# Performance work log

Hardware: AMD Instinct MI355X
Metric: run time of the kernel (lower is better)

The kernel has to match this reference:

```python
import jax, jax.numpy as jnp
import numpy as np

# Static architecture (from init_kwargs `layers`):
DAG = [0, 1, 1, 3, 3, 5]                       # parent node of linear layer i (i=1..6)
ACTS = ['tanh', 'relu', 'sigmoid', 'tanh', 'relu', 'tanh']
LEAVES = [2, 4, 6]                             # nodes never used as a parent -> combined output

V, F, H, C = 50000, 1024, 1024, 50000          # vocab, num_features, hidden_unit, num_classes
B, T = 64, 128                                 # batch, seq_len
A = 12                                         # len(actions)
N = len(DAG)


def _act(name, x):
    return {'tanh': jnp.tanh, 'relu': jax.nn.relu, 'sigmoid': jax.nn.sigmoid}[name](x)


def setup_inputs() -> dict:
    key = jax.random.key(0)
    ks = jax.random.split(key, 8)
    w = lambda k, shape: jax.random.normal(k, shape, jnp.float32) * 0.02
    return {
        'word2vec': jax.random.normal(ks[0], (V, F), jnp.float32),
        'h': jax.random.normal(ks[1], (B, H), jnp.float32),
        'batch_input': jax.random.randint(ks[2], (B, T), 0, V, jnp.int32),
        'W0': w(ks[3], (H, F)), 'b0': jnp.zeros((H,), jnp.float32),
        'Ws': w(ks[4], (N, H, H)), 'bs': jnp.zeros((N, H), jnp.float32),
        'W_out': w(ks[5], (C, H)), 'b_out': jnp.zeros((C,), jnp.float32),
        'W_sum': w(ks[6], (N, A)), 'b_sum': jnp.zeros((N,), jnp.float32),
        'actions': jnp.arange(A, dtype=jnp.float32),
    }


def reference(word2vec, h, batch_input, W0, b0, Ws, bs, W_out, b_out, W_sum, b_sum, actions):
    # softmax-weighted combine coefficients over the leaf nodes (constant across timesteps)
    weight = W_sum @ actions + b_sum                              # [N]
    clean_w = jax.nn.softmax(weight[jnp.array([l - 1 for l in LEAVES])])  # [L]

    def cell(h_t, idx):
        x = word2vec[idx]                                         # [B, F] embedding gather
        outs = {0: x @ W0.T + b0}                                 # node 0
        for i in range(1, N + 1):                                 # static DAG unroll
            prev = DAG[i - 1]
            if i == 1:
                o = h_t @ Ws[0].T + bs[0] + outs[prev]            # hidden recurrence enters node 1
            else:
                o = outs[prev] @ Ws[i - 1].T + bs[i - 1]
            outs[i] = _act(ACTS[i - 1], o)                        # dropout is identity (eval mode)
        ans = jnp.stack([outs[l] for l in LEAVES])                # [L, B, H]
        h_new = jnp.einsum('l,lbh->bh', clean_w, ans)             # weighted leaf combine
        return h_new, None

    # forward() iterates l = 1 .. T-1 (first column skipped, as in the torch code)
    h_final, _ = jax.lax.scan(cell, h, batch_input[:, 1:].T)
    return h_final @ W_out.T + b_out                              # [B, C]
```

## Files before the change

### kernel.cpp

```cpp
#include <hip/hip_runtime.h>
#include <hip/hip_bf16.h>

#define Hdim 1024
#define TST  127
#define NCLS 50000
#define POLL_GUARD (1 << 17)

typedef __attribute__((ext_vector_type(8))) short    s8v;
typedef __attribute__((ext_vector_type(4))) float    f4v;
typedef __attribute__((ext_vector_type(2))) unsigned u2v;

#define OFF_X0   0ull
#define SZ_X0    ((unsigned long long)TST * 64 * Hdim * 2ull)
#define OFF_W0B  (OFF_X0 + SZ_X0)
#define OFF_WSB  (OFF_W0B + 2097152ull)
#define OFF_ACT  (OFF_WSB + 12582912ull)
#define OFF_HB   (OFF_ACT + 524288ull)
#define OFF_FLG  (OFF_HB + 131072ull)
#define WS_NEED  (OFF_FLG + 8192ull)

__device__ __forceinline__ unsigned short f2b(float f) {
  union { float f; unsigned u; } v; v.f = f;
  return (unsigned short)((v.u + 0x7FFFu + ((v.u >> 16) & 1u)) >> 16);
}
__device__ __forceinline__ float b2f(unsigned short u) {
  union { unsigned u; float f; } v; v.u = ((unsigned)u) << 16;
  return v.f;
}
__device__ __forceinline__ float fast_tanh(float x) { return 1.f - 2.f / (__expf(2.f * x) + 1.f); }
__device__ __forceinline__ float fast_sigm(float x) { return 1.f / (1.f + __expf(-x)); }
__device__ __forceinline__ s8v pack8(const float* __restrict__ p) {
  s8v r;
#pragma unroll
  for (int i = 0; i < 8; ++i) r[i] = (short)f2b(p[i]);
  return r;
}
__device__ __forceinline__ u2v pk4(float a, float b, float c, float d) {
  u2v v;
  v[0] = (unsigned)f2b(a) | ((unsigned)f2b(b) << 16);
  v[1] = (unsigned)f2b(c) | ((unsigned)f2b(d) << 16);
  return v;
}

__device__ __forceinline__ void st_sc1_u32(unsigned* p, unsigned v) {
  asm volatile("global_store_dword %0, %1, off sc0 sc1" :: "v"(p), "v"(v) : "memory");
}
__device__ __forceinline__ void st_sc0_u32(unsigned* p, unsigned v) {
  asm volatile("global_store_dword %0, %1, off sc0" :: "v"(p), "v"(v) : "memory");
}
__device__ __forceinline__ void st_sc0_64(unsigned short* p, u2v v) {
  asm volatile("global_store_dwordx2 %0, %1, off sc0" :: "v"(p), "v"(v) : "memory");
}
__device__ __forceinline__ void wait_vm0() { asm volatile("s_waitcnt vmcnt(0)" ::: "memory"); }

__device__ __forceinline__ void pollg(const unsigned* fb, unsigned tgt) {
  const unsigned* p = fb + (threadIdx.x & 31);
  int gd = 0;
  for (;;) {
    unsigned v;
    asm volatile("global_load_dword %0, %1, off sc0 sc1\n\ts_waitcnt vmcnt(0)"
                 : "=v"(v) : "v"(p) : "memory");
    if (__all((int)(v >= tgt))) break;
    if (++gd >= POLL_GUARD) break;
  }
}

#define GL8S0(B, P) asm volatile(                                       \
  "global_load_dwordx4 %0, %8, off sc0\n\t"                             \
  "global_load_dwordx4 %1, %8, off offset:64 sc0\n\t"                   \
  "global_load_dwordx4 %2, %8, off offset:128 sc0\n\t"                  \
  "global_load_dwordx4 %3, %8, off offset:192 sc0\n\t"                  \
  "global_load_dwordx4 %4, %8, off offset:256 sc0\n\t"                  \
  "global_load_dwordx4 %5, %8, off offset:320 sc0\n\t"                  \
  "global_load_dwordx4 %6, %8, off offset:384 sc0\n\t"                  \
  "global_load_dwordx4 %7, %8, off offset:448 sc0\n\t"                  \
  "s_waitcnt vmcnt(0)"                                                  \
  : "=&v"(B[0]), "=&v"(B[1]), "=&v"(B[2]), "=&v"(B[3]),                 \
    "=&v"(B[4]), "=&v"(B[5]), "=&v"(B[6]), "=&v"(B[7])                  \
  : "v"(P) : "memory")

__global__ __launch_bounds__(256) void k_cvt(const float* __restrict__ src,
                                             unsigned short* __restrict__ dst) {
  const int i = (blockIdx.x * 256 + threadIdx.x) * 4;
  float4 v = *(const float4*)(src + i);
  ushort4 o; o.x = f2b(v.x); o.y = f2b(v.y); o.z = f2b(v.z); o.w = f2b(v.w);
  *(ushort4*)(dst + i) = o;
}

__global__ __launch_bounds__(256) void k_x0(const float* __restrict__ emb,
                                            const int* __restrict__ ids,
                                            const unsigned short* __restrict__ w0b,
                                            const float* __restrict__ b0,
                                            const float* __restrict__ bs,
                                            unsigned short* __restrict__ x0b) {
  const int t  = blockIdx.x;
  const int cb = blockIdx.y * 256;
  const int lane = threadIdx.x & 63, wvv = threadIdx.x >> 6;
  const int lc = lane & 15, lg = lane >> 4;
  const int cw = cb + wvv * 64;
  const float* erow[4];
#pragma unroll
  for (int rt = 0; rt < 4; ++rt)
    erow[rt] = emb + (size_t)ids[(rt * 16 + lc) * 128 + t + 1] * Hdim + lg * 8;
  f4v acc[4][4];
#pragma unroll
  for (int ct = 0; ct < 4; ++ct)
#pragma unroll
    for (int rt = 0; rt < 4; ++rt) acc[ct][rt] = (f4v){0.f, 0.f, 0.f, 0.f};

  for (int ks = 0; ks < 32; ++ks) {
    s8v bf[4];
#pragma unroll
    for (int rt = 0; rt < 4; ++rt) bf[rt] = pack8(erow[rt] + ks * 32);
#pragma unroll
    for (int ct = 0; ct < 4; ++ct) {
      s8v a = *(const s8v*)(w0b + (size_t)(cw + ct * 16 + lc) * Hdim + ks * 32 + lg * 8);
#pragma unroll
      for (int rt = 0; rt < 4; ++rt)
        acc[ct][rt] = __builtin_amdgcn_mfma_f32_16x16x32_bf16(a, bf[rt], acc[ct][rt], 0, 0, 0);
    }
  }
  unsigned short* xt = x0b + (size_t)t * (64 * Hdim);
#pragma unroll
  for (int ct = 0; ct < 4; ++ct) {
    const int colq = cw + ct * 16 + lg * 4;
    float4 bias = *(const float4*)(b0 + colq);
    float4 bsv  = *(const float4*)(bs + colq);
#pragma unroll
    for (int rt = 0; rt < 4; ++rt) {
      const int row = rt * 16 + lc;
      ushort4 o;
      o.x = f2b(acc[ct][rt][0] + bias.x + bsv.x);
      o.y = f2b(acc[ct][rt][1] + bias.y + bsv.y);
      o.z = f2b(acc[ct][rt][2] + bias.z + bsv.z);
      o.w = f2b(acc[ct][rt][3] + bias.w + bsv.w);
      *(ushort4*)(xt + (size_t)row * Hdim + colq) = o;
    }
  }
}

__global__ __launch_bounds__(256, 1) void k_scan(const float* __restrict__ bs,
                                                 const float* __restrict__ h_in,
                                                 const float* __restrict__ Wsum,
                                                 const float* __restrict__ bsum,
                                                 const float* __restrict__ act,
                                                 char* __restrict__ ws) {
  __shared__ float part[2][4][8][36];
  __shared__ float n2l[8][36];
  __shared__ float n4l[8][36];
  __shared__ char  pad_lds[81920];
  __shared__ int   s_info[2];

  const int tid = threadIdx.x;
  ((volatile char*)pad_lds)[tid] = (char)tid;
  asm volatile("" :: "v"((int)((volatile char*)pad_lds)[tid]));

  const int lane = tid & 63, wv = tid >> 6;
  const int lc = lane & 15, lg = lane >> 4;
  const int lr = lc & 7;
  const int lcr = lc & 7, ctx = lc >> 3;
  const int cbx = ctx * 16 + lg * 4;

  unsigned* flg_all = (unsigned*)(ws + OFF_FLG);
  unsigned* ranks   = flg_all + 1536;

  if (tid == 0) {
    unsigned x;
    asm volatile("s_getreg_b32 %0, hwreg(HW_REG_XCC_ID)" : "=s"(x));
    x &= 7u;
    unsigned rr = __hip_atomic_fetch_add(&ranks[x], 1u, __ATOMIC_RELAXED, __HIP_MEMORY_SCOPE_AGENT);
    s_info[0] = (int)x; s_info[1] = (int)rr;
  }
  __syncthreads();
  const int xcd = s_info[0];
  const int r   = s_info[1];
  if (r >= 32) return;
  const int c0w = r * 32;

  unsigned short* actX = (unsigned short*)(ws + OFF_ACT) + (size_t)xcd * 32768;
  unsigned short* hL  = actX;
  unsigned short* n1L = actX + 8192;
  unsigned short* n3L = actX + 16384;
  unsigned short* n5L = actX + 24576;
  unsigned* flgX = flg_all + xcd * 192;
  unsigned* fg0 = flgX;
  unsigned* fg2 = flgX + 64;
  unsigned* fg4 = flgX + 128;
  unsigned* fg5 = flgX + 160;
  const unsigned short* wsb = (const unsigned short*)(ws + OFF_WSB);
  const unsigned short* x0b = (const unsigned short*)(ws + OFF_X0);
  unsigned short* HB = (unsigned short*)(ws + OFF_HB);

  float cw0, cw1, cw2;
  {
    float c[3];
#pragma unroll
    for (int j = 0; j < 3; ++j) {
      const int i = 2 * j + 1;
      float s = bsum[i];
      for (int a2 = 0; a2 < 12; ++a2) s += Wsum[i * 12 + a2] * act[a2];
      c[j] = s;
    }
    float m = fmaxf(c[0], fmaxf(c[1], c[2]));
    float e0 = __expf(c[0] - m), e1 = __expf(c[1] - m), e2 = __expf(c[2] - m);
    float inv = 1.f / (e0 + e1 + e2);
    cw0 = e0 * inv; cw1 = e1 * inv; cw2 = e2 * inv;
  }

  const size_t wbase = (size_t)(c0w + lc) * Hdim + (size_t)wv * 256 + lg * 8;
  const size_t wct   = (size_t)16 * Hdim;
  s8v w1f[2][8], w2f[2][8], w3f[2][8], w4f[2][8], w5f[2][8];
#pragma unroll
  for (int i = 0; i < 8; ++i) {
    w1f[0][i] = *(const s8v*)(wsb + 1u * 1048576u + wbase + i * 32);
    w1f[1][i] = *(const s8v*)(wsb + 1u * 1048576u + wbase + wct + i * 32);
    w2f[0][i] = *(const s8v*)(wsb + 2u * 1048576u + wbase + i * 32);
    w2f[1][i] = *(const s8v*)(wsb + 2u * 1048576u + wbase + wct + i * 32);
    w3f[0][i] = *(const s8v*)(wsb + 3u * 1048576u + wbase + i * 32);
    w3f[1][i] = *(const s8v*)(wsb + 3u * 1048576u + wbase + wct + i * 32);
    w4f[0][i] = *(const s8v*)(wsb + 4u * 1048576u + wbase + i * 32);
    w4f[1][i] = *(const s8v*)(wsb + 4u * 1048576u + wbase + wct + i * 32);
    w5f[0][i] = *(const s8v*)(wsb + 5u * 1048576u + wbase + i * 32);
    w5f[1][i] = *(const s8v*)(wsb + 5u * 1048576u + wbase + wct + i * 32);
  }

  if (tid < 128) {
    const int row = tid >> 4, cp = (tid & 15) * 2;
    const float* hp = h_in + (size_t)(xcd * 8 + row) * Hdim + c0w + cp;
    unsigned pk = (unsigned)f2b(hp[0]) | ((unsigned)f2b(hp[1]) << 16);
    st_sc0_u32((unsigned*)(hL + (size_t)row * Hdim + c0w + cp), pk);
  }
  wait_vm0();
  __syncthreads();
  if (tid == 0) st_sc1_u32(fg5 + r, 1u);

  const f4v z4 = (f4v){0.f, 0.f, 0.f, 0.f};

  for (int t = 0; t < TST; ++t) {
    pollg(fg5, (unsigned)t + 1u);
    {
      s8v bb[8];
      GL8S0(bb, hL + (size_t)lr * Hdim + wv * 256 + lg * 8);
      unsigned long long w0a = (unsigned long long)wsb;
      asm volatile("" : "+v"(w0a));
      const unsigned short* w0p = (const unsigned short*)w0a;
      f4v a0 = z4, a1 = z4;
#pragma unroll
      for (int i = 0; i < 8; ++i) {
        s8v wA = *(const s8v*)(w0p + wbase + i * 32);
        s8v wB = *(const s8v*)(w0p + wbase + wct + i * 32);
        a0 = __builtin_amdgcn_mfma_f32_16x16x32_bf16(wA, bb[i], a0, 0, 0, 0);
        a1 = __builtin_amdgcn_mfma_f32_16x16x32_bf16(wB, bb[i], a1, 0, 0, 0);
      }
      if (lc < 8) {
        *(f4v*)&part[0][wv][lc][lg * 4] = a0;
        *(f4v*)&part[0][wv][lc][16 + lg * 4] = a1;
      }
    }
    __syncthreads();
    if (wv == 0) {
      f4v s = *(f4v*)&part[0][0][lcr][cbx] + *(f4v*)&part[0][1][lcr][cbx]
            + *(f4v*)&part[0][2][lcr][cbx] + *(f4v*)&part[0][3][lcr][cbx];
      ushort4 xu = *(const ushort4*)(x0b + (size_t)t * 65536 +
                                     (size_t)(xcd * 8 + lcr) * Hdim + c0w + cbx);
      st_sc0_64(n1L + (size_t)lcr * Hdim + c0w + cbx,
                pk4(fast_tanh(s[0] + b2f(xu.x)), fast_tanh(s[1] + b2f(xu.y)),
                    fast_tanh(s[2] + b2f(xu.z)), fast_tanh(s[3] + b2f(xu.w))));
      wait_vm0();
      if (lane == 0) st_sc1_u32(fg0 + r, (unsigned)t + 1u);
    }
    __syncthreads();

    pollg(fg0, (unsigned)t + 1u);
    {
      s8v bb[8];
      GL8S0(bb, n1L + (size_t)lr * Hdim + wv * 256 + lg * 8);
      f4v a20 = z4, a21 = z4, a10 = z4, a11 = z4;
#pragma unroll
      for (int i = 0; i < 8; ++i) {
        a20 = __builtin_amdgcn_mfma_f32_16x16x32_bf16(w2f[0][i], bb[i], a20, 0, 0, 0);
        a21 = __builtin_amdgcn_mfma_f32_16x16x32_bf16(w2f[1][i], bb[i], a21, 0, 0, 0);
        a10 = __builtin_amdgcn_mfma_f32_16x16x32_bf16(w1f[0][i], bb[i], a10, 0, 0, 0);
        a11 = __builtin_amdgcn_mfma_f32_16x16x32_bf16(w1f[1][i], bb[i], a11, 0, 0, 0);
      }
      if (lc < 8) {
        *(f4v*)&part[0][wv][lc][lg * 4] = a20;
        *(f4v*)&part[0][wv][lc][16 + lg * 4] = a21;
        *(f4v*)&part[1][wv][lc][lg * 4] = a10;
        *(f4v*)&part[1][wv][lc][16 + lg * 4] = a11;
      }
    }
    __syncthreads();
    if (wv == 0) {
      f4v s = *(f4v*)&part[0][0][lcr][cbx] + *(f4v*)&part[0][1][lcr][cbx]
            + *(f4v*)&part[0][2][lcr][cbx] + *(f4v*)&part[0][3][lcr][cbx];
      f4v b = *(const f4v*)(bs + 2 * Hdim + c0w + cbx);
      st_sc0_64(n3L + (size_t)lcr * Hdim + c0w + cbx,
                pk4(fast_sigm(s[0] + b[0]), fast_sigm(s[1] + b[1]),
                    fast_sigm(s[2] + b[2]), fast_sigm(s[3] + b[3])));
      wait_vm0();
      if (lane == 0) st_sc1_u32(fg2 + r, (unsigned)t + 1u);
    } else if (wv == 2) {
      f4v s = *(f4v*)&part[1][0][lcr][cbx] + *(f4v*)&part[1][1][lcr][cbx]
            + *(f4v*)&part[1][2][lcr][cbx] + *(f4v*)&part[1][3][lcr][cbx];
      f4v b = *(const f4v*)(bs + 1 * Hdim + c0w + cbx);
      f4v o; o[0] = fmaxf(s[0] + b[0], 0.f); o[1] = fmaxf(s[1] + b[1], 0.f);
             o[2] = fmaxf(s[2] + b[2], 0.f); o[3] = fmaxf(s[3] + b[3], 0.f);
      *(f4v*)&n2l[lcr][cbx] = o;
    }
    __syncthreads();

    pollg(fg2, (unsigned)t + 1u);
    {
      s8v bb[8];
      GL8S0(bb, n3L + (size_t)lr * Hdim + wv * 256 + lg * 8);
      f4v a40 = z4, a41 = z4, a30 = z4, a31 = z4;
#pragma unroll
      for (int i = 0; i < 8; ++i) {
        a40 = __builtin_amdgcn_mfma_f32_16x16x32_bf16(w4f[0][i], bb[i], a40, 0, 0, 0);
        a41 = __builtin_amdgcn_mfma_f32_16x16x32_bf16(w4f[1][i], bb[i], a41, 0, 0, 0);
        a30 = __builtin_amdgcn_mfma_f32_16x16x32_bf16(w3f[0][i], bb[i], a30, 0, 0, 0);
        a31 = __builtin_amdgcn_mfma_f32_16x16x32_bf16(w3f[1][i], bb[i], a31, 0, 0, 0);
      }
      if (lc < 8) {
        *(f4v*)&part[0][wv][lc][lg * 4] = a40;
        *(f4v*)&part[0][wv][lc][16 + lg * 4] = a41;
        *(f4v*)&part[1][wv][lc][lg * 4] = a30;
        *(f4v*)&part[1][wv][lc][16 + lg * 4] = a31;
      }
    }
    __syncthreads();
    if (wv == 0) {
      f4v s = *(f4v*)&part[0][0][lcr][cbx] + *(f4v*)&part[0][1][lcr][cbx]
            + *(f4v*)&part[0][2][lcr][cbx] + *(f4v*)&part[0][3][lcr][cbx];
      f4v b = *(const f4v*)(bs + 4 * Hdim + c0w + cbx);
      st_sc0_64(n5L + (size_t)lcr * Hdim + c0w + cbx,
                pk4(fmaxf(s[0] + b[0], 0.f), fmaxf(s[1] + b[1], 0.f),
                    fmaxf(s[2] + b[2], 0.f), fmaxf(s[3] + b[3], 0.f)));
      wait_vm0();
      if (lane == 0) st_sc1_u32(fg4 + r, (unsigned)t + 1u);
    } else if (wv == 2) {
      f4v s = *(f4v*)&part[1][0][lcr][cbx] + *(f4v*)&part[1][1][lcr][cbx]
            + *(f4v*)&part[1][2][lcr][cbx] + *(f4v*)&part[1][3][lcr][cbx];
      f4v b = *(const f4v*)(bs + 3 * Hdim + c0w + cbx);
      f4v o; o[0] = fast_tanh(s[0] + b[0]); o[1] = fast_tanh(s[1] + b[1]);
             o[2] = fast_tanh(s[2] + b[2]); o[3] = fast_tanh(s[3] + b[3]);
      *(f4v*)&n4l[lcr][cbx] = o;
    }
    __syncthreads();

    pollg(fg4, (unsigned)t + 1u);
    {
      s8v bb[8];
      GL8S0(bb, n5L + (size_t)lr * Hdim + wv * 256 + lg * 8);
      f4v a0 = z4, a1 = z4;
#pragma unroll
      for (int i = 0; i < 8; ++i) {
        a0 = __builtin_amdgcn_mfma_f32_16x16x32_bf16(w5f[0][i], bb[i], a0, 0, 0, 0);
        a1 = __builtin_amdgcn_mfma_f32_16x16x32_bf16(w5f[1][i], bb[i], a1, 0, 0, 0);
      }
      if (lc < 8) {
        *(f4v*)&part[0][wv][lc][lg * 4] = a0;
        *(f4v*)&part[0][wv][lc][16 + lg * 4] = a1;
      }
    }
    __syncthreads();
    if (wv == 0) {
      f4v s = *(f4v*)&part[0][0][lcr][cbx] + *(f4v*)&part[0][1][lcr][cbx]
            + *(f4v*)&part[0][2][lcr][cbx] + *(f4v*)&part[0][3][lcr][cbx];
      f4v b = *(const f4v*)(bs + 5 * Hdim + c0w + cbx);
      float hv[4];
#pragma unroll
      for (int j = 0; j < 4; ++j) {
        const float n6 = fast_tanh(s[j] + b[j]);
        hv[j] = cw0 * n2l[lcr][cbx + j] + cw1 * n4l[lcr][cbx + j] + cw2 * n6;
      }
      u2v pk = pk4(hv[0], hv[1], hv[2], hv[3]);
      st_sc0_64(hL + (size_t)lcr * Hdim + c0w + cbx, pk);
      if (t == TST - 1)
        *(u2v*)(HB + (size_t)(xcd * 8 + lcr) * Hdim + c0w + cbx) = pk;
      wait_vm0();
      if (lane == 0) st_sc1_u32(fg5 + r, (unsigned)t + 2u);
    }
    __syncthreads();
  }
}

__global__ __launch_bounds__(256) void k_out(const unsigned short* __restrict__ hb,
                                             const float* __restrict__ wout,
                                             const float* __restrict__ bout,
                                             float* __restrict__ out) {
  const int cb = blockIdx.x * 128;
  const int lane = threadIdx.x & 63, wvv = threadIdx.x >> 6;
  const int lc = lane & 15, lg = lane >> 4;
  const int cw = cb + wvv * 32;
  f4v acc[4][2];
#pragma unroll
  for (int rt = 0; rt < 4; ++rt)
#pragma unroll
    for (int ct = 0; ct < 2; ++ct) acc[rt][ct] = (f4v){0.f, 0.f, 0.f, 0.f};

  for (int ks = 0; ks < 32; ++ks) {
    s8v a[4];
#pragma unroll
    for (int rt = 0; rt < 4; ++rt)
      a[rt] = *(const s8v*)(hb + (rt * 16 + lc) * Hdim + ks * 32 + lg * 8);
#pragma unroll
    for (int ct = 0; ct < 2; ++ct) {
      const int col = cw + ct * 16 + lc;
      const int cs = col < NCLS ? col : NCLS - 1;
      s8v b = pack8(wout + (size_t)cs * Hdim + ks * 32 + lg * 8);
#pragma unroll
      for (int rt = 0; rt < 4; ++rt)
        acc[rt][ct] = __builtin_amdgcn_mfma_f32_16x16x32_bf16(a[rt], b, acc[rt][ct], 0, 0, 0);
    }
  }
#pragma unroll
  for (int ct = 0; ct < 2; ++ct) {
    const int col = cw + ct * 16 + lc;
    if (col < NCLS) {
      const float bias = bout[col];
#pragma unroll
      for (int rt = 0; rt < 4; ++rt)
#pragma unroll
        for (int j = 0; j < 4; ++j)
          out[(size_t)(rt * 16 + lg * 4 + j) * NCLS + col] = acc[rt][ct][j] + bias;
    }
  }
}

extern "C" void kernel_launch(void* const* d_in, const int* in_sizes, int n_in,
                              void* d_out, int out_size, void* d_ws, size_t ws_size,
                              hipStream_t stream) {
  (void)in_sizes; (void)n_in; (void)out_size;
  if (ws_size < WS_NEED) return;

  const float* emb  = (const float*)d_in[0];
  const float* h0   = (const float*)d_in[1];
  const int*   ids  = (const int*)d_in[2];
  const float* W0   = (const float*)d_in[3];
  const float* b0   = (const float*)d_in[4];
  const float* Ws   = (const float*)d_in[5];
  const float* bsp  = (const float*)d_in[6];
  const float* Wout = (const float*)d_in[7];
  const float* bout = (const float*)d_in[8];
  const float* Wsum = (const float*)d_in[9];
  const float* bsum = (const float*)d_in[10];
  const float* actv = (const float*)d_in[11];
  char* ws  = (char*)d_ws;
  float* out = (float*)d_out;

  hipMemsetAsync(ws + OFF_FLG, 0, 8192, stream);
  k_cvt<<<1024, 256, 0, stream>>>(W0, (unsigned short*)(ws + OFF_W0B));
  k_cvt<<<6144, 256, 0, stream>>>(Ws, (unsigned short*)(ws + OFF_WSB));
  k_x0<<<dim3(TST, 4), 256, 0, stream>>>(emb, ids, (const unsigned short*)(ws + OFF_W0B),
                                         b0, bsp, (unsigned short*)(ws + OFF_X0));

  void* args[] = { (void*)&bsp, (void*)&h0, (void*)&Wsum,
                   (void*)&bsum, (void*)&actv, (void*)&ws };
  hipError_t e = hipLaunchCooperativeKernel((void*)k_scan, dim3(256), dim3(256), args, 0, stream);
  if (e != hipSuccess) {
    k_scan<<<dim3(256), dim3(256), 0, stream>>>(bsp, h0, Wsum, bsum, actv, ws);
  }

  k_out<<<391, 256, 0, stream>>>((const unsigned short*)(ws + OFF_HB), Wout, bout, out);
}
```

Baseline: 1.795 ms.

## Use per-wave flags and distributed epilogue to drop block barriers in scan

Each of the four waves in a block now finalises its own slice of output columns and publishes its own completion flag, in place of wave 0 (and wave 2) doing the epilogue and then a block-wide barrier before signalling. Pollers read 128 flags with 64-bit loads across 64 lanes. The intermediate n2/n4 values are kept in registers per wave rather than in shared LDS arrays. Part buffers are double-indexed so consecutive stages don't collide without the trailing barrier. This removes one __syncthreads per stage and spreads the epilogue work, at the cost of four times as many flags to poll per step.

```diff
diff --git a/kernel.cpp b/kernel.cpp
--- a/kernel.cpp
+++ b/kernel.cpp
@@ -17,7 +17,7 @@
 #define OFF_ACT  (OFF_WSB + 12582912ull)
 #define OFF_HB   (OFF_ACT + 524288ull)
 #define OFF_FLG  (OFF_HB + 131072ull)
-#define WS_NEED  (OFF_FLG + 8192ull)
+#define WS_NEED  (OFF_FLG + 16448ull)
 
 __device__ __forceinline__ unsigned short f2b(float f) {
   union { float f; unsigned u; } v; v.f = f;
@@ -53,14 +53,14 @@
 }
 __device__ __forceinline__ void wait_vm0() { asm volatile("s_waitcnt vmcnt(0)" ::: "memory"); }
 
-__device__ __forceinline__ void pollg(const unsigned* fb, unsigned tgt) {
-  const unsigned* p = fb + (threadIdx.x & 31);
+__device__ __forceinline__ void pollg64(const unsigned long long* fb, unsigned tgt) {
+  const unsigned long long* p = fb + (threadIdx.x & 63);
   int gd = 0;
   for (;;) {
-    unsigned v;
-    asm volatile("global_load_dword %0, %1, off sc0 sc1\n\ts_waitcnt vmcnt(0)"
+    unsigned long long v;
+    asm volatile("global_load_dwordx2 %0, %1, off sc0 sc1\n\ts_waitcnt vmcnt(0)"
                  : "=v"(v) : "v"(p) : "memory");
-    if (__all((int)(v >= tgt))) break;
+    if (__all((int)(((unsigned)v >= tgt) & ((unsigned)(v >> 32) >= tgt)))) break;
     if (++gd >= POLL_GUARD) break;
   }
 }
@@ -145,10 +145,8 @@
                                                  const float* __restrict__ bsum,
                                                  const float* __restrict__ act,
                                                  char* __restrict__ ws) {
-  __shared__ float part[2][4][8][36];
-  __shared__ float n2l[8][36];
-  __shared__ float n4l[8][36];
-  __shared__ char  pad_lds[81920];
+  __shared__ float part[2][2][4][8][36];
+  __shared__ char  pad_lds[49152];
   __shared__ int   s_info[2];
 
   const int tid = threadIdx.x;
@@ -158,11 +156,11 @@
   const int lane = tid & 63, wv = tid >> 6;
   const int lc = lane & 15, lg = lane >> 4;
   const int lr = lc & 7;
-  const int lcr = lc & 7, ctx = lc >> 3;
-  const int cbx = ctx * 16 + lg * 4;
+  const int lr2 = lane & 7, q = (lane >> 3) & 1;
+  const int co = wv * 8 + q * 4;
 
   unsigned* flg_all = (unsigned*)(ws + OFF_FLG);
-  unsigned* ranks   = flg_all + 1536;
+  unsigned* ranks   = flg_all + 4096;
 
   if (tid == 0) {
     unsigned x;
@@ -176,17 +174,18 @@
   const int r   = s_info[1];
   if (r >= 32) return;
   const int c0w = r * 32;
+  const int fidx = r * 4 + wv;
 
   unsigned short* actX = (unsigned short*)(ws + OFF_ACT) + (size_t)xcd * 32768;
   unsigned short* hL  = actX;
   unsigned short* n1L = actX + 8192;
   unsigned short* n3L = actX + 16384;
   unsigned short* n5L = actX + 24576;
-  unsigned* flgX = flg_all + xcd * 192;
-  unsigned* fg0 = flgX;
-  unsigned* fg2 = flgX + 64;
-  unsigned* fg4 = flgX + 128;
-  unsigned* fg5 = flgX + 160;
+  unsigned* flgX = flg_all + xcd * 512;
+  unsigned* gn1 = flgX;
+  unsigned* gn3 = flgX + 128;
+  unsigned* gn5 = flgX + 256;
+  unsigned* gh  = flgX + 384;
   const unsigned short* wsb = (const unsigned short*)(ws + OFF_WSB);
   const unsigned short* x0b = (const unsigned short*)(ws + OFF_X0);
   unsigned short* HB = (unsigned short*)(ws + OFF_HB);
@@ -232,12 +231,14 @@
   }
   wait_vm0();
   __syncthreads();
-  if (tid == 0) st_sc1_u32(fg5 + r, 1u);
+  if (lane == 0) st_sc1_u32(gh + fidx, 1u);
 
   const f4v z4 = (f4v){0.f, 0.f, 0.f, 0.f};
+  f4v n2reg = z4, n4reg = z4;
 
   for (int t = 0; t < TST; ++t) {
-    pollg(fg5, (unsigned)t + 1u);
+    const unsigned tq = (unsigned)t + 1u;
+    pollg64((const unsigned long long*)gh, tq);
     {
       s8v bb[8];
       GL8S0(bb, hL + (size_t)lr * Hdim + wv * 256 + lg * 8);
@@ -253,25 +254,24 @@
         a1 = __builtin_amdgcn_mfma_f32_16x16x32_bf16(wB, bb[i], a1, 0, 0, 0);
       }
       if (lc < 8) {
-        *(f4v*)&part[0][wv][lc][lg * 4] = a0;
-        *(f4v*)&part[0][wv][lc][16 + lg * 4] = a1;
+        *(f4v*)&part[0][0][wv][lc][lg * 4] = a0;
+        *(f4v*)&part[0][0][wv][lc][16 + lg * 4] = a1;
       }
     }
     __syncthreads();
-    if (wv == 0) {
-      f4v s = *(f4v*)&part[0][0][lcr][cbx] + *(f4v*)&part[0][1][lcr][cbx]
-            + *(f4v*)&part[0][2][lcr][cbx] + *(f4v*)&part[0][3][lcr][cbx];
+    if (lane < 16) {
+      f4v s = *(f4v*)&part[0][0][0][lr2][co] + *(f4v*)&part[0][0][1][lr2][co]
+            + *(f4v*)&part[0][0][2][lr2][co] + *(f4v*)&part[0][0][3][lr2][co];
       ushort4 xu = *(const ushort4*)(x0b + (size_t)t * 65536 +
-                                     (size_t)(xcd * 8 + lcr) * Hdim + c0w + cbx);
-      st_sc0_64(n1L + (size_t)lcr * Hdim + c0w + cbx,
+                                     (size_t)(xcd * 8 + lr2) * Hdim + c0w + co);
+      st_sc0_64(n1L + (size_t)lr2 * Hdim + c0w + co,
                 pk4(fast_tanh(s[0] + b2f(xu.x)), fast_tanh(s[1] + b2f(xu.y)),
                     fast_tanh(s[2] + b2f(xu.z)), fast_tanh(s[3] + b2f(xu.w))));
-      wait_vm0();
-      if (lane == 0) st_sc1_u32(fg0 + r, (unsigned)t + 1u);
-    }
-    __syncthreads();
-
-    pollg(fg0, (unsigned)t + 1u);
+    }
+    wait_vm0();
+    if (lane == 0) st_sc1_u32(gn1 + fidx, tq);
+
+    pollg64((const unsigned long long*)gn1, tq);
     {
       s8v bb[8];
       GL8S0(bb, n1L + (size_t)lr * Hdim + wv * 256 + lg * 8);
@@ -284,33 +284,30 @@
         a11 = __builtin_amdgcn_mfma_f32_16x16x32_bf16(w1f[1][i], bb[i], a11, 0, 0, 0);
       }
       if (lc < 8) {
-        *(f4v*)&part[0][wv][lc][lg * 4] = a20;
-        *(f4v*)&part[0][wv][lc][16 + lg * 4] = a21;
-        *(f4v*)&part[1][wv][lc][lg * 4] = a10;
-        *(f4v*)&part[1][wv][lc][16 + lg * 4] = a11;
+        *(f4v*)&part[1][0][wv][lc][lg * 4] = a20;
+        *(f4v*)&part[1][0][wv][lc][16 + lg * 4] = a21;
+        *(f4v*)&part[1][1][wv][lc][lg * 4] = a10;
+        *(f4v*)&part[1][1][wv][lc][16 + lg * 4] = a11;
       }
     }
     __syncthreads();
-    if (wv == 0) {
-      f4v s = *(f4v*)&part[0][0][lcr][cbx] + *(f4v*)&part[0][1][lcr][cbx]
-            + *(f4v*)&part[0][2][lcr][cbx] + *(f4v*)&part[0][3][lcr][cbx];
-      f4v b = *(const f4v*)(bs + 2 * Hdim + c0w + cbx);
-      st_sc0_64(n3L + (size_t)lcr * Hdim + c0w + cbx,
-                pk4(fast_sigm(s[0] + b[0]), fast_sigm(s[1] + b[1]),
-                    fast_sigm(s[2] + b[2]), fast_sigm(s[3] + b[3])));
-      wait_vm0();
-      if (lane == 0) st_sc1_u32(fg2 + r, (unsigned)t + 1u);
-    } else if (wv == 2) {
-      f4v s = *(f4v*)&part[1][0][lcr][cbx] + *(f4v*)&part[1][1][lcr][cbx]
-            + *(f4v*)&part[1][2][lcr][cbx] + *(f4v*)&part[1][3][lcr][cbx];
-      f4v b = *(const f4v*)(bs + 1 * Hdim + c0w + cbx);
-      f4v o; o[0] = fmaxf(s[0] + b[0], 0.f); o[1] = fmaxf(s[1] + b[1], 0.f);
-             o[2] = fmaxf(s[2] + b[2], 0.f); o[3] = fmaxf(s[3] + b[3], 0.f);
-      *(f4v*)&n2l[lcr][cbx] = o;
-    }
-    __syncthreads();
-
-    pollg(fg2, (unsigned)t + 1u);
+    if (lane < 16) {
+      f4v s3 = *(f4v*)&part[1][0][0][lr2][co] + *(f4v*)&part[1][0][1][lr2][co]
+             + *(f4v*)&part[1][0][2][lr2][co] + *(f4v*)&part[1][0][3][lr2][co];
+      f4v s2 = *(f4v*)&part[1][1][0][lr2][co] + *(f4v*)&part[1][1][1][lr2][co]
+             + *(f4v*)&part[1][1][2][lr2][co] + *(f4v*)&part[1][1][3][lr2][co];
+      f4v b3 = *(const f4v*)(bs + 2 * Hdim + c0w + co);
+      f4v b2 = *(const f4v*)(bs + 1 * Hdim + c0w + co);
+      st_sc0_64(n3L + (size_t)lr2 * Hdim + c0w + co,
+                pk4(fast_sigm(s3[0] + b3[0]), fast_sigm(s3[1] + b3[1]),
+                    fast_sigm(s3[2] + b3[2]), fast_sigm(s3[3] + b3[3])));
+      n2reg[0] = fmaxf(s2[0] + b2[0], 0.f); n2reg[1] = fmaxf(s2[1] + b2[1], 0.f);
+      n2reg[2] = fmaxf(s2[2] + b2[2], 0.f); n2reg[3] = fmaxf(s2[3] + b2[3], 0.f);
+    }
+    wait_vm0();
+    if (lane == 0) st_sc1_u32(gn3 + fidx, tq);
+
+    pollg64((const unsigned long long*)gn3, tq);
     {
       s8v bb[8];
       GL8S0(bb, n3L + (size_t)lr * Hdim + wv * 256 + lg * 8);
@@ -323,33 +320,30 @@
         a31 = __builtin_amdgcn_mfma_f32_16x16x32_bf16(w3f[1][i], bb[i], a31, 0, 0, 0);
       }
       if (lc < 8) {
-        *(f4v*)&part[0][wv][lc][lg * 4] = a40;
-        *(f4v*)&part[0][wv][lc][16 + lg * 4] = a41;
-        *(f4v*)&part[1][wv][lc][lg * 4] = a30;
-        *(f4v*)&part[1][wv][lc][16 + lg * 4] = a31;
+        *(f4v*)&part[0][0][wv][lc][lg * 4] = a40;
+        *(f4v*)&part[0][0][wv][lc][16 + lg * 4] = a41;
+        *(f4v*)&part[0][1][wv][lc][lg * 4] = a30;
+        *(f4v*)&part[0][1][wv][lc][16 + lg * 4] = a31;
       }
     }
     __syncthreads();
-    if (wv == 0) {
-      f4v s = *(f4v*)&part[0][0][lcr][cbx] + *(f4v*)&part[0][1][lcr][cbx]
-            + *(f4v*)&part[0][2][lcr][cbx] + *(f4v*)&part[0][3][lcr][cbx];
-      f4v b = *(const f4v*)(bs + 4 * Hdim + c0w + cbx);
-      st_sc0_64(n5L + (size_t)lcr * Hdim + c0w + cbx,
-                pk4(fmaxf(s[0] + b[0], 0.f), fmaxf(s[1] + b[1], 0.f),
-                    fmaxf(s[2] + b[2], 0.f), fmaxf(s[3] + b[3], 0.f)));
-      wait_vm0();
-      if (lane == 0) st_sc1_u32(fg4 + r, (unsigned)t + 1u);
-    } else if (wv == 2) {
-      f4v s = *(f4v*)&part[1][0][lcr][cbx] + *(f4v*)&part[1][1][lcr][cbx]
-            + *(f4v*)&part[1][2][lcr][cbx] + *(f4v*)&part[1][3][lcr][cbx];
-      f4v b = *(const f4v*)(bs + 3 * Hdim + c0w + cbx);
-      f4v o; o[0] = fast_tanh(s[0] + b[0]); o[1] = fast_tanh(s[1] + b[1]);
-             o[2] = fast_tanh(s[2] + b[2]); o[3] = fast_tanh(s[3] + b[3]);
-      *(f4v*)&n4l[lcr][cbx] = o;
-    }
-    __syncthreads();
-
-    pollg(fg4, (unsigned)t + 1u);
+    if (lane < 16) {
+      f4v s5 = *(f4v*)&part[0][0][0][lr2][co] + *(f4v*)&part[0][0][1][lr2][co]
+             + *(f4v*)&part[0][0][2][lr2][co] + *(f4v*)&part[0][0][3][lr2][co];
+      f4v s4 = *(f4v*)&part[0][1][0][lr2][co] + *(f4v*)&part[0][1][1][lr2][co]
+             + *(f4v*)&part[0][1][2][lr2][co] + *(f4v*)&part[0][1][3][lr2][co];
+      f4v b5 = *(const f4v*)(bs + 4 * Hdim + c0w + co);
+      f4v b4 = *(const f4v*)(bs + 3 * Hdim + c0w + co);
+      st_sc0_64(n5L + (size_t)lr2 * Hdim + c0w + co,
+                pk4(fmaxf(s5[0] + b5[0], 0.f), fmaxf(s5[1] + b5[1], 0.f),
+                    fmaxf(s5[2] + b5[2], 0.f), fmaxf(s5[3] + b5[3], 0.f)));
+      n4reg[0] = fast_tanh(s4[0] + b4[0]); n4reg[1] = fast_tanh(s4[1] + b4[1]);
+      n4reg[2] = fast_tanh(s4[2] + b4[2]); n4reg[3] = fast_tanh(s4[3] + b4[3]);
+    }
+    wait_vm0();
+    if (lane == 0) st_sc1_u32(gn5 + fidx, tq);
+
+    pollg64((const unsigned long long*)gn5, tq);
     {
       s8v bb[8];
       GL8S0(bb, n5L + (size_t)lr * Hdim + wv * 256 + lg * 8);
@@ -360,29 +354,28 @@
         a1 = __builtin_amdgcn_mfma_f32_16x16x32_bf16(w5f[1][i], bb[i], a1, 0, 0, 0);
       }
       if (lc < 8) {
-        *(f4v*)&part[0][wv][lc][lg * 4] = a0;
-        *(f4v*)&part[0][wv][lc][16 + lg * 4] = a1;
+        *(f4v*)&part[1][0][wv][lc][lg * 4] = a0;
+        *(f4v*)&part[1][0][wv][lc][16 + lg * 4] = a1;
       }
     }
     __syncthreads();
-    if (wv == 0) {
-      f4v s = *(f4v*)&part[0][0][lcr][cbx] + *(f4v*)&part[0][1][lcr][cbx]
-            + *(f4v*)&part[0][2][lcr][cbx] + *(f4v*)&part[0][3][lcr][cbx];
-      f4v b = *(const f4v*)(bs + 5 * Hdim + c0w + cbx);
+    if (lane < 16) {
+      f4v s = *(f4v*)&part[1][0][0][lr2][co] + *(f4v*)&part[1][0][1][lr2][co]
+            + *(f4v*)&part[1][0][2][lr2][co] + *(f4v*)&part[1][0][3][lr2][co];
+      f4v b6 = *(const f4v*)(bs + 5 * Hdim + c0w + co);
       float hv[4];
 #pragma unroll
       for (int j = 0; j < 4; ++j) {
-        const float n6 = fast_tanh(s[j] + b[j]);
-        hv[j] = cw0 * n2l[lcr][cbx + j] + cw1 * n4l[lcr][cbx + j] + cw2 * n6;
+        const float n6 = fast_tanh(s[j] + b6[j]);
+        hv[j] = cw0 * n2reg[j] + cw1 * n4reg[j] + cw2 * n6;
       }
       u2v pk = pk4(hv[0], hv[1], hv[2], hv[3]);
-      st_sc0_64(hL + (size_t)lcr * Hdim + c0w + cbx, pk);
+      st_sc0_64(hL + (size_t)lr2 * Hdim + c0w + co, pk);
       if (t == TST - 1)
-        *(u2v*)(HB + (size_t)(xcd * 8 + lcr) * Hdim + c0w + cbx) = pk;
-      wait_vm0();
-      if (lane == 0) st_sc1_u32(fg5 + r, (unsigned)t + 2u);
-    }
-    __syncthreads();
+        *(u2v*)(HB + (size_t)(xcd * 8 + lr2) * Hdim + c0w + co) = pk;
+    }
+    wait_vm0();
+    if (lane == 0) st_sc1_u32(gh + fidx, tq + 1u);
   }
 }
 
@@ -450,7 +443,7 @@
   char* ws  = (char*)d_ws;
   float* out = (float*)d_out;
 
-  hipMemsetAsync(ws + OFF_FLG, 0, 8192, stream);
+  hipMemsetAsync(ws + OFF_FLG, 0, 16448, stream);
   k_cvt<<<1024, 256, 0, stream>>>(W0, (unsigned short*)(ws + OFF_W0B));
   k_cvt<<<6144, 256, 0, stream>>>(Ws, (unsigned short*)(ws + OFF_WSB));
   k_x0<<<dim3(TST, 4), 256, 0, stream>>>(emb, ids, (const unsigned short*)(ws + OFF_W0B),
```

Measured after the change: 3.781 ms. 2.11x slower.

## Split per-XCD batch into two 4-row chunks to pipeline DAG stages

Applied to the files above, without the earlier changes.

Each XCD's 8 batch rows are split into two independent 4-row chunks, each with its own activation buffers and flag sets. Each DAG stage runs chunk 0 then chunk 1, so chunk 0's flag can be signalled while chunk 1 computes. This is meant to hide inter-block polling latency behind useful work. The cost is twice as many syncs, polls and MFMA passes, with half of each MFMA tile's rows unused.

```diff
diff --git a/kernel.cpp b/kernel.cpp
--- a/kernel.cpp
+++ b/kernel.cpp
@@ -17,7 +17,7 @@
 #define OFF_ACT  (OFF_WSB + 12582912ull)
 #define OFF_HB   (OFF_ACT + 524288ull)
 #define OFF_FLG  (OFF_HB + 131072ull)
-#define WS_NEED  (OFF_FLG + 8192ull)
+#define WS_NEED  (OFF_FLG + 16448ull)
 
 __device__ __forceinline__ unsigned short f2b(float f) {
   union { float f; unsigned u; } v; v.f = f;
@@ -146,8 +146,8 @@
                                                  const float* __restrict__ act,
                                                  char* __restrict__ ws) {
   __shared__ float part[2][4][8][36];
-  __shared__ float n2l[8][36];
-  __shared__ float n4l[8][36];
+  __shared__ float n2l[2][4][36];
+  __shared__ float n4l[2][4][36];
   __shared__ char  pad_lds[81920];
   __shared__ int   s_info[2];
 
@@ -157,12 +157,10 @@
 
   const int lane = tid & 63, wv = tid >> 6;
   const int lc = lane & 15, lg = lane >> 4;
-  const int lr = lc & 7;
-  const int lcr = lc & 7, ctx = lc >> 3;
-  const int cbx = ctx * 16 + lg * 4;
+  const int lr4 = lc & 3;
 
   unsigned* flg_all = (unsigned*)(ws + OFF_FLG);
-  unsigned* ranks   = flg_all + 1536;
+  unsigned* ranks   = flg_all + 2048;
 
   if (tid == 0) {
     unsigned x;
@@ -178,15 +176,7 @@
   const int c0w = r * 32;
 
   unsigned short* actX = (unsigned short*)(ws + OFF_ACT) + (size_t)xcd * 32768;
-  unsigned short* hL  = actX;
-  unsigned short* n1L = actX + 8192;
-  unsigned short* n3L = actX + 16384;
-  unsigned short* n5L = actX + 24576;
-  unsigned* flgX = flg_all + xcd * 192;
-  unsigned* fg0 = flgX;
-  unsigned* fg2 = flgX + 64;
-  unsigned* fg4 = flgX + 128;
-  unsigned* fg5 = flgX + 160;
+  unsigned* flgX = flg_all + xcd * 256;
   const unsigned short* wsb = (const unsigned short*)(ws + OFF_WSB);
   const unsigned short* x0b = (const unsigned short*)(ws + OFF_X0);
   unsigned short* HB = (unsigned short*)(ws + OFF_HB);
@@ -225,164 +215,207 @@
   }
 
   if (tid < 128) {
-    const int row = tid >> 4, cp = (tid & 15) * 2;
-    const float* hp = h_in + (size_t)(xcd * 8 + row) * Hdim + c0w + cp;
+    const int c = tid >> 6, row4 = (tid >> 4) & 3, cp = (tid & 15) * 2;
+    const float* hp = h_in + (size_t)(xcd * 8 + c * 4 + row4) * Hdim + c0w + cp;
     unsigned pk = (unsigned)f2b(hp[0]) | ((unsigned)f2b(hp[1]) << 16);
-    st_sc0_u32((unsigned*)(hL + (size_t)row * Hdim + c0w + cp), pk);
+    st_sc0_u32((unsigned*)(actX + (size_t)c * 16384 + (size_t)row4 * Hdim + c0w + cp), pk);
   }
   wait_vm0();
   __syncthreads();
-  if (tid == 0) st_sc1_u32(fg5 + r, 1u);
+  if (tid == 0) {
+    st_sc1_u32(flgX + 0 * 128 + 96 + r, 1u);
+    st_sc1_u32(flgX + 1 * 128 + 96 + r, 1u);
+  }
 
   const f4v z4 = (f4v){0.f, 0.f, 0.f, 0.f};
 
   for (int t = 0; t < TST; ++t) {
-    pollg(fg5, (unsigned)t + 1u);
-    {
-      s8v bb[8];
-      GL8S0(bb, hL + (size_t)lr * Hdim + wv * 256 + lg * 8);
-      unsigned long long w0a = (unsigned long long)wsb;
-      asm volatile("" : "+v"(w0a));
-      const unsigned short* w0p = (const unsigned short*)w0a;
-      f4v a0 = z4, a1 = z4;
-#pragma unroll
-      for (int i = 0; i < 8; ++i) {
-        s8v wA = *(const s8v*)(w0p + wbase + i * 32);
-        s8v wB = *(const s8v*)(w0p + wbase + wct + i * 32);
-        a0 = __builtin_amdgcn_mfma_f32_16x16x32_bf16(wA, bb[i], a0, 0, 0, 0);
-        a1 = __builtin_amdgcn_mfma_f32_16x16x32_bf16(wB, bb[i], a1, 0, 0, 0);
-      }
-      if (lc < 8) {
-        *(f4v*)&part[0][wv][lc][lg * 4] = a0;
-        *(f4v*)&part[0][wv][lc][16 + lg * 4] = a1;
-      }
-    }
-    __syncthreads();
-    if (wv == 0) {
-      f4v s = *(f4v*)&part[0][0][lcr][cbx] + *(f4v*)&part[0][1][lcr][cbx]
-            + *(f4v*)&part[0][2][lcr][cbx] + *(f4v*)&part[0][3][lcr][cbx];
-      ushort4 xu = *(const ushort4*)(x0b + (size_t)t * 65536 +
-                                     (size_t)(xcd * 8 + lcr) * Hdim + c0w + cbx);
-      st_sc0_64(n1L + (size_t)lcr * Hdim + c0w + cbx,
-                pk4(fast_tanh(s[0] + b2f(xu.x)), fast_tanh(s[1] + b2f(xu.y)),
-                    fast_tanh(s[2] + b2f(xu.z)), fast_tanh(s[3] + b2f(xu.w))));
-      wait_vm0();
-      if (lane == 0) st_sc1_u32(fg0 + r, (unsigned)t + 1u);
-    }
-    __syncthreads();
-
-    pollg(fg0, (unsigned)t + 1u);
-    {
-      s8v bb[8];
-      GL8S0(bb, n1L + (size_t)lr * Hdim + wv * 256 + lg * 8);
-      f4v a20 = z4, a21 = z4, a10 = z4, a11 = z4;
-#pragma unroll
-      for (int i = 0; i < 8; ++i) {
-        a20 = __builtin_amdgcn_mfma_f32_16x16x32_bf16(w2f[0][i], bb[i], a20, 0, 0, 0);
-        a21 = __builtin_amdgcn_mfma_f32_16x16x32_bf16(w2f[1][i], bb[i], a21, 0, 0, 0);
-        a10 = __builtin_amdgcn_mfma_f32_16x16x32_bf16(w1f[0][i], bb[i], a10, 0, 0, 0);
-        a11 = __builtin_amdgcn_mfma_f32_16x16x32_bf16(w1f[1][i], bb[i], a11, 0, 0, 0);
-      }
-      if (lc < 8) {
-        *(f4v*)&part[0][wv][lc][lg * 4] = a20;
-        *(f4v*)&part[0][wv][lc][16 + lg * 4] = a21;
-        *(f4v*)&part[1][wv][lc][lg * 4] = a10;
-        *(f4v*)&part[1][wv][lc][16 + lg * 4] = a11;
-      }
-    }
-    __syncthreads();
-    if (wv == 0) {
-      f4v s = *(f4v*)&part[0][0][lcr][cbx] + *(f4v*)&part[0][1][lcr][cbx]
-            + *(f4v*)&part[0][2][lcr][cbx] + *(f4v*)&part[0][3][lcr][cbx];
-      f4v b = *(const f4v*)(bs + 2 * Hdim + c0w + cbx);
-      st_sc0_64(n3L + (size_t)lcr * Hdim + c0w + cbx,
-                pk4(fast_sigm(s[0] + b[0]), fast_sigm(s[1] + b[1]),
-                    fast_sigm(s[2] + b[2]), fast_sigm(s[3] + b[3])));
-      wait_vm0();
-      if (lane == 0) st_sc1_u32(fg2 + r, (unsigned)t + 1u);
-    } else if (wv == 2) {
-      f4v s = *(f4v*)&part[1][0][lcr][cbx] + *(f4v*)&part[1][1][lcr][cbx]
-            + *(f4v*)&part[1][2][lcr][cbx] + *(f4v*)&part[1][3][lcr][cbx];
-      f4v b = *(const f4v*)(bs + 1 * Hdim + c0w + cbx);
-      f4v o; o[0] = fmaxf(s[0] + b[0], 0.f); o[1] = fmaxf(s[1] + b[1], 0.f);
-             o[2] = fmaxf(s[2] + b[2], 0.f); o[3] = fmaxf(s[3] + b[3], 0.f);
-      *(f4v*)&n2l[lcr][cbx] = o;
-    }
-    __syncthreads();
-
-    pollg(fg2, (unsigned)t + 1u);
-    {
-      s8v bb[8];
-      GL8S0(bb, n3L + (size_t)lr * Hdim + wv * 256 + lg * 8);
-      f4v a40 = z4, a41 = z4, a30 = z4, a31 = z4;
-#pragma unroll
-      for (int i = 0; i < 8; ++i) {
-        a40 = __builtin_amdgcn_mfma_f32_16x16x32_bf16(w4f[0][i], bb[i], a40, 0, 0, 0);
-        a41 = __builtin_amdgcn_mfma_f32_16x16x32_bf16(w4f[1][i], bb[i], a41, 0, 0, 0);
-        a30 = __builtin_amdgcn_mfma_f32_16x16x32_bf16(w3f[0][i], bb[i], a30, 0, 0, 0);
-        a31 = __builtin_amdgcn_mfma_f32_16x16x32_bf16(w3f[1][i], bb[i], a31, 0, 0, 0);
-      }
-      if (lc < 8) {
-        *(f4v*)&part[0][wv][lc][lg * 4] = a40;
-        *(f4v*)&part[0][wv][lc][16 + lg * 4] = a41;
-        *(f4v*)&part[1][wv][lc][lg * 4] = a30;
-        *(f4v*)&part[1][wv][lc][16 + lg * 4] = a31;
-      }
-    }
-    __syncthreads();
-    if (wv == 0) {
-      f4v s = *(f4v*)&part[0][0][lcr][cbx] + *(f4v*)&part[0][1][lcr][cbx]
-            + *(f4v*)&part[0][2][lcr][cbx] + *(f4v*)&part[0][3][lcr][cbx];
-      f4v b = *(const f4v*)(bs + 4 * Hdim + c0w + cbx);
-      st_sc0_64(n5L + (size_t)lcr * Hdim + c0w + cbx,
-                pk4(fmaxf(s[0] + b[0], 0.f), fmaxf(s[1] + b[1], 0.f),
-                    fmaxf(s[2] + b[2], 0.f), fmaxf(s[3] + b[3], 0.f)));
-      wait_vm0();
-      if (lane == 0) st_sc1_u32(fg4 + r, (unsigned)t + 1u);
-    } else if (wv == 2) {
-      f4v s = *(f4v*)&part[1][0][lcr][cbx] + *(f4v*)&part[1][1][lcr][cbx]
-            + *(f4v*)&part[1][2][lcr][cbx] + *(f4v*)&part[1][3][lcr][cbx];
-      f4v b = *(const f4v*)(bs + 3 * Hdim + c0w + cbx);
-      f4v o; o[0] = fast_tanh(s[0] + b[0]); o[1] = fast_tanh(s[1] + b[1]);
-             o[2] = fast_tanh(s[2] + b[2]); o[3] = fast_tanh(s[3] + b[3]);
-      *(f4v*)&n4l[lcr][cbx] = o;
-    }
-    __syncthreads();
-
-    pollg(fg4, (unsigned)t + 1u);
-    {
-      s8v bb[8];
-      GL8S0(bb, n5L + (size_t)lr * Hdim + wv * 256 + lg * 8);
-      f4v a0 = z4, a1 = z4;
-#pragma unroll
-      for (int i = 0; i < 8; ++i) {
-        a0 = __builtin_amdgcn_mfma_f32_16x16x32_bf16(w5f[0][i], bb[i], a0, 0, 0, 0);
-        a1 = __builtin_amdgcn_mfma_f32_16x16x32_bf16(w5f[1][i], bb[i], a1, 0, 0, 0);
-      }
-      if (lc < 8) {
-        *(f4v*)&part[0][wv][lc][lg * 4] = a0;
-        *(f4v*)&part[0][wv][lc][16 + lg * 4] = a1;
-      }
-    }
-    __syncthreads();
-    if (wv == 0) {
-      f4v s = *(f4v*)&part[0][0][lcr][cbx] + *(f4v*)&part[0][1][lcr][cbx]
-            + *(f4v*)&part[0][2][lcr][cbx] + *(f4v*)&part[0][3][lcr][cbx];
-      f4v b = *(const f4v*)(bs + 5 * Hdim + c0w + cbx);
-      float hv[4];
-#pragma unroll
-      for (int j = 0; j < 4; ++j) {
-        const float n6 = fast_tanh(s[j] + b[j]);
-        hv[j] = cw0 * n2l[lcr][cbx + j] + cw1 * n4l[lcr][cbx + j] + cw2 * n6;
-      }
-      u2v pk = pk4(hv[0], hv[1], hv[2], hv[3]);
-      st_sc0_64(hL + (size_t)lcr * Hdim + c0w + cbx, pk);
-      if (t == TST - 1)
-        *(u2v*)(HB + (size_t)(xcd * 8 + lcr) * Hdim + c0w + cbx) = pk;
-      wait_vm0();
-      if (lane == 0) st_sc1_u32(fg5 + r, (unsigned)t + 2u);
-    }
-    __syncthreads();
+    const unsigned tq = (unsigned)t + 1u;
+
+#pragma unroll
+    for (int c = 0; c < 2; ++c) {
+      unsigned short* actC = actX + (size_t)c * 16384;
+      unsigned* fgc = flgX + c * 128;
+      pollg(fgc + 96, tq);
+      {
+        s8v bb[8];
+        GL8S0(bb, actC + (size_t)lr4 * Hdim + wv * 256 + lg * 8);
+        unsigned long long w0a = (unsigned long long)wsb;
+        asm volatile("" : "+v"(w0a));
+        const unsigned short* w0p = (const unsigned short*)w0a;
+        f4v a0 = z4, a1 = z4;
+#pragma unroll
+        for (int i = 0; i < 8; ++i) {
+          s8v wA = *(const s8v*)(w0p + wbase + i * 32);
+          s8v wB = *(const s8v*)(w0p + wbase + wct + i * 32);
+          a0 = __builtin_amdgcn_mfma_f32_16x16x32_bf16(wA, bb[i], a0, 0, 0, 0);
+          a1 = __builtin_amdgcn_mfma_f32_16x16x32_bf16(wB, bb[i], a1, 0, 0, 0);
+        }
+        if (lc < 4) {
+          *(f4v*)&part[0][wv][lc][lg * 4] = a0;
+          *(f4v*)&part[0][wv][lc][16 + lg * 4] = a1;
+        }
+      }
+      __syncthreads();
+      if (wv == 0) {
+        if (lane < 32) {
+          const int rrow = lane & 3, co = (lane >> 2) * 4;
+          f4v s = *(f4v*)&part[0][0][rrow][co] + *(f4v*)&part[0][1][rrow][co]
+                + *(f4v*)&part[0][2][rrow][co] + *(f4v*)&part[0][3][rrow][co];
+          ushort4 xu = *(const ushort4*)(x0b + (size_t)t * 65536 +
+                                         (size_t)(xcd * 8 + c * 4 + rrow) * Hdim + c0w + co);
+          st_sc0_64(actC + 4096 + (size_t)rrow * Hdim + c0w + co,
+                    pk4(fast_tanh(s[0] + b2f(xu.x)), fast_tanh(s[1] + b2f(xu.y)),
+                        fast_tanh(s[2] + b2f(xu.z)), fast_tanh(s[3] + b2f(xu.w))));
+        }
+        wait_vm0();
+        if (lane == 0) st_sc1_u32(fgc + 0 + r, tq);
+      }
+      __syncthreads();
+    }
+
+#pragma unroll
+    for (int c = 0; c < 2; ++c) {
+      unsigned short* actC = actX + (size_t)c * 16384;
+      unsigned* fgc = flgX + c * 128;
+      pollg(fgc + 0, tq);
+      {
+        s8v bb[8];
+        GL8S0(bb, actC + 4096 + (size_t)lr4 * Hdim + wv * 256 + lg * 8);
+        f4v a20 = z4, a21 = z4, a10 = z4, a11 = z4;
+#pragma unroll
+        for (int i = 0; i < 8; ++i) {
+          a20 = __builtin_amdgcn_mfma_f32_16x16x32_bf16(w2f[0][i], bb[i], a20, 0, 0, 0);
+          a21 = __builtin_amdgcn_mfma_f32_16x16x32_bf16(w2f[1][i], bb[i], a21, 0, 0, 0);
+          a10 = __builtin_amdgcn_mfma_f32_16x16x32_bf16(w1f[0][i], bb[i], a10, 0, 0, 0);
+          a11 = __builtin_amdgcn_mfma_f32_16x16x32_bf16(w1f[1][i], bb[i], a11, 0, 0, 0);
+        }
+        if (lc < 4) {
+          *(f4v*)&part[0][wv][lc][lg * 4] = a20;
+          *(f4v*)&part[0][wv][lc][16 + lg * 4] = a21;
+          *(f4v*)&part[1][wv][lc][lg * 4] = a10;
+          *(f4v*)&part[1][wv][lc][16 + lg * 4] = a11;
+        }
+      }
+      __syncthreads();
+      if (wv == 0) {
+        if (lane < 32) {
+          const int rrow = lane & 3, co = (lane >> 2) * 4;
+          f4v s3 = *(f4v*)&part[0][0][rrow][co] + *(f4v*)&part[0][1][rrow][co]
+                 + *(f4v*)&part[0][2][rrow][co] + *(f4v*)&part[0][3][rrow][co];
+          f4v b3 = *(const f4v*)(bs + 2 * Hdim + c0w + co);
+          st_sc0_64(actC + 8192 + (size_t)rrow * Hdim + c0w + co,
+                    pk4(fast_sigm(s3[0] + b3[0]), fast_sigm(s3[1] + b3[1]),
+                        fast_sigm(s3[2] + b3[2]), fast_sigm(s3[3] + b3[3])));
+        }
+        wait_vm0();
+        if (lane == 0) st_sc1_u32(fgc + 32 + r, tq);
+      } else if (wv == 2) {
+        if (lane < 32) {
+          const int rrow = lane & 3, co = (lane >> 2) * 4;
+          f4v s2 = *(f4v*)&part[1][0][rrow][co] + *(f4v*)&part[1][1][rrow][co]
+                 + *(f4v*)&part[1][2][rrow][co] + *(f4v*)&part[1][3][rrow][co];
+          f4v b2 = *(const f4v*)(bs + 1 * Hdim + c0w + co);
+          f4v o; o[0] = fmaxf(s2[0] + b2[0], 0.f); o[1] = fmaxf(s2[1] + b2[1], 0.f);
+                 o[2] = fmaxf(s2[2] + b2[2], 0.f); o[3] = fmaxf(s2[3] + b2[3], 0.f);
+          *(f4v*)&n2l[c][rrow][co] = o;
+        }
+      }
+      __syncthreads();
+    }
+
+#pragma unroll
+    for (int c = 0; c < 2; ++c) {
+      unsigned short* actC = actX + (size_t)c * 16384;
+      unsigned* fgc = flgX + c * 128;
+      pollg(fgc + 32, tq);
+      {
+        s8v bb[8];
+        GL8S0(bb, actC + 8192 + (size_t)lr4 * Hdim + wv * 256 + lg * 8);
+        f4v a40 = z4, a41 = z4, a30 = z4, a31 = z4;
+#pragma unroll
+        for (int i = 0; i < 8; ++i) {
+          a40 = __builtin_amdgcn_mfma_f32_16x16x32_bf16(w4f[0][i], bb[i], a40, 0, 0, 0);
+          a41 = __builtin_amdgcn_mfma_f32_16x16x32_bf16(w4f[1][i], bb[i], a41, 0, 0, 0);
+          a30 = __builtin_amdgcn_mfma_f32_16x16x32_bf16(w3f[0][i], bb[i], a30, 0, 0, 0);
+          a31 = __builtin_amdgcn_mfma_f32_16x16x32_bf16(w3f[1][i], bb[i], a31, 0, 0, 0);
+        }
+        if (lc < 4) {
+          *(f4v*)&part[0][wv][lc][lg * 4] = a40;
+          *(f4v*)&part[0][wv][lc][16 + lg * 4] = a41;
+          *(f4v*)&part[1][wv][lc][lg * 4] = a30;
+          *(f4v*)&part[1][wv][lc][16 + lg * 4] = a31;
+        }
+      }
+      __syncthreads();
+      if (wv == 0) {
+        if (lane < 32) {
+          const int rrow = lane & 3, co = (lane >> 2) * 4;
+          f4v s5 = *(f4v*)&part[0][0][rrow][co] + *(f4v*)&part[0][1][rrow][co]
+                 + *(f4v*)&part[0][2][rrow][co] + *(f4v*)&part[0][3][rrow][co];
+          f4v b5 = *(const f4v*)(bs + 4 * Hdim + c0w + co);
+          st_sc0_64(actC + 12288 + (size_t)rrow * Hdim + c0w + co,
+                    pk4(fmaxf(s5[0] + b5[0], 0.f), fmaxf(s5[1] + b5[1], 0.f),
+                        fmaxf(s5[2] + b5[2], 0.f), fmaxf(s5[3] + b5[3], 0.f)));
+        }
+        wait_vm0();
+        if (lane == 0) st_sc1_u32(fgc + 64 + r, tq);
+      } else if (wv == 2) {
+        if (lane < 32) {
+          const int rrow = lane & 3, co = (lane >> 2) * 4;
+          f4v s4 = *(f4v*)&part[1][0][rrow][co] + *(f4v*)&part[1][1][rrow][co]
+                 + *(f4v*)&part[1][2][rrow][co] + *(f4v*)&part[1][3][rrow][co];
+          f4v b4 = *(const f4v*)(bs + 3 * Hdim + c0w + co);
+          f4v o; o[0] = fast_tanh(s4[0] + b4[0]); o[1] = fast_tanh(s4[1] + b4[1]);
+                 o[2] = fast_tanh(s4[2] + b4[2]); o[3] = fast_tanh(s4[3] + b4[3]);
+          *(f4v*)&n4l[c][rrow][co] = o;
+        }
+      }
+      __syncthreads();
+    }
+
+#pragma unroll
+    for (int c = 0; c < 2; ++c) {
+      unsigned short* actC = actX + (size_t)c * 16384;
+      unsigned* fgc = flgX + c * 128;
+      pollg(fgc + 64, tq);
+      {
+        s8v bb[8];
+        GL8S0(bb, actC + 12288 + (size_t)lr4 * Hdim + wv * 256 + lg * 8);
+        f4v a0 = z4, a1 = z4;
+#pragma unroll
+        for (int i = 0; i < 8; ++i) {
+          a0 = __builtin_amdgcn_mfma_f32_16x16x32_bf16(w5f[0][i], bb[i], a0, 0, 0, 0);
+          a1 = __builtin_amdgcn_mfma_f32_16x16x32_bf16(w5f[1][i], bb[i], a1, 0, 0, 0);
+        }
+        if (lc < 4) {
+          *(f4v*)&part[0][wv][lc][lg * 4] = a0;
+          *(f4v*)&part[0][wv][lc][16 + lg * 4] = a1;
+        }
+      }
+      __syncthreads();
+      if (wv == 0) {
+        if (lane < 32) {
+          const int rrow = lane & 3, co = (lane >> 2) * 4;
+          f4v s = *(f4v*)&part[0][0][rrow][co] + *(f4v*)&part[0][1][rrow][co]
+                + *(f4v*)&part[0][2][rrow][co] + *(f4v*)&part[0][3][rrow][co];
+          f4v b6 = *(const f4v*)(bs + 5 * Hdim + c0w + co);
+          float hv[4];
+#pragma unroll
+          for (int j = 0; j < 4; ++j) {
+            const float n6 = fast_tanh(s[j] + b6[j]);
+            hv[j] = cw0 * n2l[c][rrow][co + j] + cw1 * n4l[c][rrow][co + j] + cw2 * n6;
+          }
+          u2v pk = pk4(hv[0], hv[1], hv[2], hv[3]);
+          st_sc0_64(actC + (size_t)rrow * Hdim + c0w + co, pk);
+          if (t == TST - 1)
+            *(u2v*)(HB + (size_t)(xcd * 8 + c * 4 + rrow) * Hdim + c0w + co) = pk;
+        }
+        wait_vm0();
+        if (lane == 0) st_sc1_u32(fgc + 96 + r, tq + 1u);
+      }
+      __syncthreads();
+    }
   }
 }
 
@@ -450,7 +483,7 @@
   char* ws  = (char*)d_ws;
   float* out = (float*)d_out;
 
-  hipMemsetAsync(ws + OFF_FLG, 0, 8192, stream);
+  hipMemsetAsync(ws + OFF_FLG, 0, 16448, stream);
   k_cvt<<<1024, 256, 0, stream>>>(W0, (unsigned short*)(ws + OFF_W0B));
   k_cvt<<<6144, 256, 0, stream>>>(Ws, (unsigned short*)(ws + OFF_WSB));
   k_x0<<<dim3(TST, 4), 256, 0, stream>>>(emb, ids, (const unsigned short*)(ws + OFF_W0B),
```

Result: slower. 2.793 ms (+55.6%).
